# Optimization experiments

Hardware: AMD Instinct MI355X
Metric: run time of the kernel (lower is better)

The kernel has to match this reference:

```python
import jax, jax.numpy as jnp
import numpy as np

B, S, H, E, K = 4, 2048, 1024, 8, 2

def setup_inputs() -> dict:
    key = jax.random.key(0)
    k0, k1, k2, k3 = jax.random.split(key, 4)
    x = jax.random.normal(k0, (B, S, H), dtype=jnp.float32)
    # xavier-uniform-like scales
    router_w = jax.random.normal(k1, (E, H), dtype=jnp.float32) * np.float32(1.0 / np.sqrt(H))
    xav1 = np.float32(np.sqrt(2.0 / (2 * H + H)))
    w1 = jax.random.normal(k2, (E, 2 * H, H), dtype=jnp.float32) * xav1
    w2 = jax.random.normal(k3, (E, H, 2 * H), dtype=jnp.float32) * xav1
    return {"x": x, "router_w": router_w, "w1": w1, "w2": w2}

def reference(x, router_w, w1, w2):
    bsz, seq, hidden = x.shape
    n_experts = w1.shape[0]
    tokens = x.reshape(-1, hidden)                      # [T, H]
    T = tokens.shape[0]
    logits = tokens @ router_w.T                        # [T, E]
    topv, topi = jax.lax.top_k(logits, K)               # [T, K]
    w = jax.nn.softmax(topv, axis=-1).astype(tokens.dtype)
    # Dense gate matrix: gate[t, e] = routing weight of expert e for token t
    # (zero for non-selected experts). Equivalent to the torch pad/dispatch/
    # scatter-add combine: padded slots have weight 0 and contribute nothing.
    gate = jnp.zeros((T, n_experts), tokens.dtype).at[jnp.arange(T)[:, None], topi].add(w)
    out = jnp.zeros_like(tokens)
    for e in range(n_experts):  # small fixed expert count
        h = jax.nn.gelu(tokens @ w1[e].T, approximate=False)  # [T, 2H] (torch F.gelu = erf)
        y = h @ w2[e].T                                       # [T, H]
        out = out + gate[:, e:e + 1] * y
    return out.reshape(bsz, seq, hidden)
```

## Files before the change

### kernel.cpp

```cpp
#include <hip/hip_runtime.h>
#include <stdint.h>
#include <math.h>

#define T_TOK 8192
#define H_DIM 1024
#define H2    2048
#define NE    8

typedef unsigned short u16;
typedef __attribute__((ext_vector_type(8))) short bf16x8;
typedef __attribute__((ext_vector_type(4))) float f32x4;

__device__ __forceinline__ u16 f32_to_bf16(float f) {
  union { float f; unsigned u; } c; c.f = f;
  unsigned u = c.u + 0x7fffu + ((c.u >> 16) & 1u);
  return (u16)(u >> 16);
}
__device__ __forceinline__ float bf2f(u16 v) {
  union { unsigned u; float f; } c; c.u = (unsigned)v << 16; return c.f;
}

__device__ __forceinline__ float fast_gelu(float v) {
  float u = v * v;
  float z2 = v * fmaf(u, 0.1029437f, 2.3022078f);
  float e = __builtin_amdgcn_exp2f(z2);
  float r = __builtin_amdgcn_rcpf(1.0f + e);
  return v - v * r;
}

__device__ __forceinline__ void g2l16(const void* g, void* l) {
  __builtin_amdgcn_global_load_lds(
      (const __attribute__((address_space(1))) unsigned*)g,
      (__attribute__((address_space(3))) unsigned*)l, 16, 0, 0);
}

__device__ __forceinline__ int prefix_base(const int* counts, int e) {
  int b = 0;
#pragma unroll
  for (int j = 0; j < NE; j++) b += (j < e) ? counts[j] : 0;
  return b;
}

__global__ __launch_bounds__(256) void prep_kernel(
    const float* __restrict__ x, const float* __restrict__ rw,
    const float* __restrict__ w1, const float* __restrict__ w2,
    u16* __restrict__ xb, u16* __restrict__ w1b, u16* __restrict__ w2b,
    int* __restrict__ tope, float2* __restrict__ gate2,
    int* __restrict__ counts) {
  int blk = blockIdx.x;
  if (blk < T_TOK / 4) {
    int wave = threadIdx.x >> 6;
    int lane = threadIdx.x & 63;
    int t = blk * 4 + wave;
    const float4* x4 = (const float4*)(x + (size_t)t * H_DIM);
    const float4* rw4 = (const float4*)rw;
    u16* xbrow = xb + (size_t)t * H_DIM;

    double acc[NE];
#pragma unroll
    for (int e = 0; e < NE; e++) acc[e] = 0.0;
#pragma unroll
    for (int i = 0; i < 4; i++) {
      int c = lane + 64 * i;
      float4 xv = x4[c];
      ushort4 bv = make_ushort4(f32_to_bf16(xv.x), f32_to_bf16(xv.y),
                                f32_to_bf16(xv.z), f32_to_bf16(xv.w));
      *(ushort4*)(xbrow + c * 4) = bv;
#pragma unroll
      for (int e = 0; e < NE; e++) {
        float4 wv = rw4[e * 256 + c];
        acc[e] += (double)xv.x * wv.x + (double)xv.y * wv.y +
                  (double)xv.z * wv.z + (double)xv.w * wv.w;
      }
    }
#pragma unroll
    for (int off = 32; off >= 1; off >>= 1)
#pragma unroll
      for (int e = 0; e < NE; e++) acc[e] += __shfl_xor(acc[e], off, 64);

    if (lane == 0) {
      int e0 = 0; double v0 = acc[0];
#pragma unroll
      for (int e = 1; e < NE; e++) if (acc[e] > v0) { v0 = acc[e]; e0 = e; }
      int e1 = -1; double v1 = -1e300;
#pragma unroll
      for (int e = 0; e < NE; e++) if (e != e0 && acc[e] > v1) { v1 = acc[e]; e1 = e; }
      double ex = exp(v1 - v0);
      tope[t] = e0 | (e1 << 8);
      gate2[t] = make_float2((float)(1.0 / (1.0 + ex)), (float)(ex / (1.0 + ex)));
    }
  } else {
    int cb = blk - T_TOK / 4;
    if (cb == 0 && threadIdx.x < NE) counts[threadIdx.x] = 0;
    const float* src; u16* dst;
    if (cb < 3072) { src = w1; dst = w1b; }
    else           { src = w2; dst = w2b; cb -= 3072; }
    const int n4 = NE * H2 * H_DIM / 4;
    const int stride = 3072 * 256;
    const float4* s4 = (const float4*)src;
    for (int i = cb * 256 + threadIdx.x; i < n4; i += stride) {
      float4 v = s4[i];
      *(ushort4*)(dst + (size_t)i * 4) = make_ushort4(
          f32_to_bf16(v.x), f32_to_bf16(v.y), f32_to_bf16(v.z), f32_to_bf16(v.w));
    }
  }
}

__global__ __launch_bounds__(256) void build_kernel(
    const int* __restrict__ tope, int* __restrict__ counts,
    int* __restrict__ tok_list, int2* __restrict__ pos2) {
  __shared__ int cts[4][NE];
  __shared__ int gbase[NE];
  int tid = threadIdx.x, lane = tid & 63, w = tid >> 6;
  int t = blockIdx.x * 256 + tid;
  int pk = tope[t];
  int e0 = pk & 0xff, e1 = (pk >> 8) & 0xff;
  unsigned long long lt = ((unsigned long long)1 << lane) - 1;

  int r0 = 0, r1 = 0;
#pragma unroll
  for (int e = 0; e < NE; e++) {
    unsigned long long b0 = __ballot(e0 == e);
    unsigned long long b1 = __ballot(e1 == e);
    int n0 = __popcll(b0), n1 = __popcll(b1);
    if (e0 == e) r0 = __popcll(b0 & lt);
    if (e1 == e) r1 = n0 + __popcll(b1 & lt);
    if (lane == 0) cts[w][e] = n0 + n1;
  }
  __syncthreads();
  if (tid < NE) {
    int bt = cts[0][tid] + cts[1][tid] + cts[2][tid] + cts[3][tid];
    gbase[tid] = atomicAdd(&counts[tid], bt);
  }
  __syncthreads();
  int off0 = gbase[e0] + r0;
  int off1 = gbase[e1] + r1;
#pragma unroll
  for (int wp = 0; wp < 4; wp++) {
    if (wp < w) { off0 += cts[wp][e0]; off1 += cts[wp][e1]; }
  }
  tok_list[e0 * T_TOK + off0] = t;
  tok_list[e1 * T_TOK + off1] = t;
  pos2[t] = make_int2(off0, off1);
}

template <int NKT, int NT, int OUTN, bool GATHER, bool GELU>
__global__ __launch_bounds__(512, 2) void moe_gemm(
    const u16* __restrict__ A, const u16* __restrict__ W,
    u16* __restrict__ O, const int* __restrict__ tok_list,
    const int* __restrict__ counts) {
  int e = blockIdx.x & 7;
  int rem = blockIdx.x >> 3;
  int mt = rem / NT, nt = rem % NT;
  int cnt = counts[e];
  int m0 = mt * 256;
  if (m0 >= cnt) return;
  int base = prefix_base(counts, e);
  const int K = NKT * 64;

  __shared__ u16 lA[2][16384];
  __shared__ u16 lB[2][16384];

  int tid = threadIdx.x;
  int ln = tid & 63, w = tid >> 6;
  int wr = w >> 2, wc = w & 3;
  int quad = ln >> 4, l16 = ln & 15;

  const u16* We = W + (size_t)e * OUTN * K;
  const u16* aptr[4]; const u16* bptr[4];
#pragma unroll
  for (int c = 0; c < 4; ++c) {
    int u = c * 512 + tid;
    int row = u >> 3;
    int chunk = (u & 7) ^ (row & 7);
    int ar = m0 + row; if (ar > cnt - 1) ar = cnt - 1;
    const u16* ab;
    if (GATHER) ab = A + (size_t)tok_list[e * T_TOK + ar] * K;
    else        ab = A + (size_t)(base + ar) * K;
    aptr[c] = ab + chunk * 8;
    bptr[c] = We + (size_t)(nt * 256 + row) * K + chunk * 8;
  }

  int adA[8][2], adB[4][2];
#pragma unroll
  for (int f = 0; f < 8; ++f) {
    int r = wr * 128 + f * 16 + l16;
#pragma unroll
    for (int kk = 0; kk < 2; ++kk)
      adA[f][kk] = r * 64 + ((((kk << 2) | quad) ^ (r & 7)) << 3);
  }
#pragma unroll
  for (int j = 0; j < 4; ++j) {
    int r = wc * 64 + j * 16 + l16;
#pragma unroll
    for (int kk = 0; kk < 2; ++kk)
      adB[j][kk] = r * 64 + ((((kk << 2) | quad) ^ (r & 7)) << 3);
  }

  f32x4 acc[8][4];
#pragma unroll
  for (int i = 0; i < 8; i++)
#pragma unroll
    for (int j = 0; j < 4; j++)
#pragma unroll
      for (int r = 0; r < 4; r++) acc[i][j][r] = 0.f;

#pragma unroll
  for (int c = 0; c < 4; ++c) {
    g2l16(aptr[c], &lA[0][(c * 512 + tid) * 8]);
    g2l16(bptr[c], &lB[0][(c * 512 + tid) * 8]);
  }

#pragma unroll 1
  for (int t = 0; t < NKT; ++t) {
    int d = t & 1;
    asm volatile("s_waitcnt vmcnt(0)" ::: "memory");
    __builtin_amdgcn_s_barrier();
    __builtin_amdgcn_sched_barrier(0);

    const u16* Ab = &lA[d][0];
    const u16* Bb = &lB[d][0];
    bf16x8 af[8], af2[8], bf[4], bf2v[4];
    af[0]  = *(const bf16x8*)(Ab + adA[0][0]);
    af2[0] = *(const bf16x8*)(Ab + adA[0][1]);
#pragma unroll
    for (int j = 0; j < 4; ++j) {
      bf[j]   = *(const bf16x8*)(Bb + adB[j][0]);
      bf2v[j] = *(const bf16x8*)(Bb + adB[j][1]);
    }
#pragma unroll
    for (int f = 1; f < 8; ++f) {
      af[f]  = *(const bf16x8*)(Ab + adA[f][0]);
      af2[f] = *(const bf16x8*)(Ab + adA[f][1]);
    }

    if (t + 1 < NKT) {
#pragma unroll
      for (int c = 0; c < 4; ++c) {
        g2l16(aptr[c] + (t + 1) * 64, &lA[d ^ 1][(c * 512 + tid) * 8]);
        g2l16(bptr[c] + (t + 1) * 64, &lB[d ^ 1][(c * 512 + tid) * 8]);
      }
    }
    __builtin_amdgcn_sched_barrier(0);

    __builtin_amdgcn_s_setprio(1);
#pragma unroll
    for (int mi = 0; mi < 8; ++mi) {
#pragma unroll
      for (int ni = 0; ni < 4; ++ni)
        acc[mi][ni] = __builtin_amdgcn_mfma_f32_16x16x32_bf16(
            af[mi], bf[ni], acc[mi][ni], 0, 0, 0);
#pragma unroll
      for (int ni = 0; ni < 4; ++ni)
        acc[mi][ni] = __builtin_amdgcn_mfma_f32_16x16x32_bf16(
            af2[mi], bf2v[ni], acc[mi][ni], 0, 0, 0);
    }
    __builtin_amdgcn_s_setprio(0);
  }

#pragma unroll
  for (int mi = 0; mi < 8; ++mi) {
    int rb = wr * 128 + mi * 16 + quad * 4;
#pragma unroll
    for (int r = 0; r < 4; ++r) {
      int grow = m0 + rb + r;
      if (grow < cnt) {
        size_t o = (size_t)(base + grow) * OUTN + nt * 256 + wc * 64 + l16;
#pragma unroll
        for (int ni = 0; ni < 4; ++ni) {
          float v = acc[mi][ni][r];
          if (GELU) v = fast_gelu(v);
          O[o + ni * 16] = f32_to_bf16(v);
        }
      }
    }
  }
}

__global__ __launch_bounds__(256) void combine_kernel(
    const u16* __restrict__ y, const int* __restrict__ tope,
    const float2* __restrict__ gate2, const int2* __restrict__ pos2,
    const int* __restrict__ counts, float* __restrict__ out) {
  int t = blockIdx.x;
  int pk = tope[t];
  int e0 = pk & 0xff, e1 = (pk >> 8) & 0xff;
  float2 g = gate2[t];
  int2 p = pos2[t];
  int hb0 = prefix_base(counts, e0);
  int hb1 = prefix_base(counts, e1);
  size_t s0 = (size_t)(hb0 + p.x) * H_DIM + threadIdx.x * 4;
  size_t s1 = (size_t)(hb1 + p.y) * H_DIM + threadIdx.x * 4;
  ushort4 a = *(const ushort4*)(y + s0);
  ushort4 b = *(const ushort4*)(y + s1);
  float4 o;
  o.x = g.x * bf2f(a.x) + g.y * bf2f(b.x);
  o.y = g.x * bf2f(a.y) + g.y * bf2f(b.y);
  o.z = g.x * bf2f(a.z) + g.y * bf2f(b.z);
  o.w = g.x * bf2f(a.w) + g.y * bf2f(b.w);
  *(float4*)(out + (size_t)t * H_DIM + threadIdx.x * 4) = o;
}

extern "C" void kernel_launch(void* const* d_in, const int* in_sizes, int n_in,
                              void* d_out, int out_size, void* d_ws, size_t ws_size,
                              hipStream_t stream) {
  const float* x  = (const float*)d_in[0];
  const float* rw = (const float*)d_in[1];
  const float* w1 = (const float*)d_in[2];
  const float* w2 = (const float*)d_in[3];
  float* out = (float*)d_out;

  char* ws = (char*)d_ws;
  u16* xb       = (u16*)(ws);
  u16* w1b      = (u16*)(ws + 16777216);
  u16* y        = (u16*)(ws + 16777216);
  u16* w2b      = (u16*)(ws + 50331648);
  u16* h        = (u16*)(ws + 83886080);
  int* tok_list = (int*)(ws + 150994944);
  int* tope     = (int*)(ws + 151257088);
  float2* gate2 = (float2*)(ws + 151289856);
  int2* pos2    = (int2*)(ws + 151355392);
  int* counts   = (int*)(ws + 151420928);

  prep_kernel<<<T_TOK / 4 + 6144, 256, 0, stream>>>(x, rw, w1, w2, xb, w1b, w2b,
                                                    tope, gate2, counts);
  build_kernel<<<T_TOK / 256, 256, 0, stream>>>(tope, counts, tok_list, pos2);
  moe_gemm<16, 8, H2, true, true>
      <<<NE * 32 * 8, 512, 0, stream>>>(xb, w1b, h, tok_list, counts);
  moe_gemm<32, 4, H_DIM, false, false>
      <<<NE * 32 * 4, 512, 0, stream>>>(h, w2b, y, tok_list, counts);
  combine_kernel<<<T_TOK, 256, 0, stream>>>(y, tope, gate2, pos2, counts, out);
}
```

Before: 390.7 us.

## Fuse fp32-to-bf16 weight conversion into GEMM loads and split-K second GEMM

Drops the separate pass that converted w1/w2 to bf16. Each GEMM now reads fp32 weights directly into registers, packs them to bf16 and writes them into swizzled LDS, with the store deferred until after the MFMAs so it overlaps compute. The second GEMM is split into two K halves written to separate buffers, and the combine kernel sums both halves. This avoids writing and rereading bf16 weight copies and doubles the block count of the second GEMM, at the cost of fp32 weight traffic inside the GEMMs, extra partial-output traffic, and register pressure.

```diff
diff --git a/kernel.cpp b/kernel.cpp
--- a/kernel.cpp
+++ b/kernel.cpp
@@ -18,6 +18,12 @@
 }
 __device__ __forceinline__ float bf2f(u16 v) {
   union { unsigned u; float f; } c; c.u = (unsigned)v << 16; return c.f;
+}
+__device__ __forceinline__ unsigned pk_bf16(float lo, float hi) {
+  union { float f; unsigned u; } a, b; a.f = lo; b.f = hi;
+  unsigned ua = a.u + 0x7fffu + ((a.u >> 16) & 1u);
+  unsigned ub = b.u + 0x7fffu + ((b.u >> 16) & 1u);
+  return (ua >> 16) | (ub & 0xffff0000u);
 }
 
 __device__ __forceinline__ float fast_gelu(float v) {
@@ -43,66 +49,49 @@
 
 __global__ __launch_bounds__(256) void prep_kernel(
     const float* __restrict__ x, const float* __restrict__ rw,
-    const float* __restrict__ w1, const float* __restrict__ w2,
-    u16* __restrict__ xb, u16* __restrict__ w1b, u16* __restrict__ w2b,
-    int* __restrict__ tope, float2* __restrict__ gate2,
+    u16* __restrict__ xb, int* __restrict__ tope, float2* __restrict__ gate2,
     int* __restrict__ counts) {
   int blk = blockIdx.x;
-  if (blk < T_TOK / 4) {
-    int wave = threadIdx.x >> 6;
-    int lane = threadIdx.x & 63;
-    int t = blk * 4 + wave;
-    const float4* x4 = (const float4*)(x + (size_t)t * H_DIM);
-    const float4* rw4 = (const float4*)rw;
-    u16* xbrow = xb + (size_t)t * H_DIM;
-
-    double acc[NE];
-#pragma unroll
-    for (int e = 0; e < NE; e++) acc[e] = 0.0;
-#pragma unroll
-    for (int i = 0; i < 4; i++) {
-      int c = lane + 64 * i;
-      float4 xv = x4[c];
-      ushort4 bv = make_ushort4(f32_to_bf16(xv.x), f32_to_bf16(xv.y),
-                                f32_to_bf16(xv.z), f32_to_bf16(xv.w));
-      *(ushort4*)(xbrow + c * 4) = bv;
-#pragma unroll
-      for (int e = 0; e < NE; e++) {
-        float4 wv = rw4[e * 256 + c];
-        acc[e] += (double)xv.x * wv.x + (double)xv.y * wv.y +
-                  (double)xv.z * wv.z + (double)xv.w * wv.w;
-      }
-    }
-#pragma unroll
-    for (int off = 32; off >= 1; off >>= 1)
-#pragma unroll
-      for (int e = 0; e < NE; e++) acc[e] += __shfl_xor(acc[e], off, 64);
-
-    if (lane == 0) {
-      int e0 = 0; double v0 = acc[0];
-#pragma unroll
-      for (int e = 1; e < NE; e++) if (acc[e] > v0) { v0 = acc[e]; e0 = e; }
-      int e1 = -1; double v1 = -1e300;
-#pragma unroll
-      for (int e = 0; e < NE; e++) if (e != e0 && acc[e] > v1) { v1 = acc[e]; e1 = e; }
-      double ex = exp(v1 - v0);
-      tope[t] = e0 | (e1 << 8);
-      gate2[t] = make_float2((float)(1.0 / (1.0 + ex)), (float)(ex / (1.0 + ex)));
-    }
-  } else {
-    int cb = blk - T_TOK / 4;
-    if (cb == 0 && threadIdx.x < NE) counts[threadIdx.x] = 0;
-    const float* src; u16* dst;
-    if (cb < 3072) { src = w1; dst = w1b; }
-    else           { src = w2; dst = w2b; cb -= 3072; }
-    const int n4 = NE * H2 * H_DIM / 4;
-    const int stride = 3072 * 256;
-    const float4* s4 = (const float4*)src;
-    for (int i = cb * 256 + threadIdx.x; i < n4; i += stride) {
-      float4 v = s4[i];
-      *(ushort4*)(dst + (size_t)i * 4) = make_ushort4(
-          f32_to_bf16(v.x), f32_to_bf16(v.y), f32_to_bf16(v.z), f32_to_bf16(v.w));
-    }
+  if (blk == 0 && threadIdx.x < NE) counts[threadIdx.x] = 0;
+  int wave = threadIdx.x >> 6;
+  int lane = threadIdx.x & 63;
+  int t = blk * 4 + wave;
+  const float4* x4 = (const float4*)(x + (size_t)t * H_DIM);
+  const float4* rw4 = (const float4*)rw;
+  u16* xbrow = xb + (size_t)t * H_DIM;
+
+  double acc[NE];
+#pragma unroll
+  for (int e = 0; e < NE; e++) acc[e] = 0.0;
+#pragma unroll
+  for (int i = 0; i < 4; i++) {
+    int c = lane + 64 * i;
+    float4 xv = x4[c];
+    ushort4 bv = make_ushort4(f32_to_bf16(xv.x), f32_to_bf16(xv.y),
+                              f32_to_bf16(xv.z), f32_to_bf16(xv.w));
+    *(ushort4*)(xbrow + c * 4) = bv;
+#pragma unroll
+    for (int e = 0; e < NE; e++) {
+      float4 wv = rw4[e * 256 + c];
+      acc[e] += (double)xv.x * wv.x + (double)xv.y * wv.y +
+                (double)xv.z * wv.z + (double)xv.w * wv.w;
+    }
+  }
+#pragma unroll
+  for (int off = 32; off >= 1; off >>= 1)
+#pragma unroll
+    for (int e = 0; e < NE; e++) acc[e] += __shfl_xor(acc[e], off, 64);
+
+  if (lane == 0) {
+    int e0 = 0; double v0 = acc[0];
+#pragma unroll
+    for (int e = 1; e < NE; e++) if (acc[e] > v0) { v0 = acc[e]; e0 = e; }
+    int e1 = -1; double v1 = -1e300;
+#pragma unroll
+    for (int e = 0; e < NE; e++) if (e != e0 && acc[e] > v1) { v1 = acc[e]; e1 = e; }
+    double ex = exp(v1 - v0);
+    tope[t] = e0 | (e1 << 8);
+    gate2[t] = make_float2((float)(1.0 / (1.0 + ex)), (float)(ex / (1.0 + ex)));
   }
 }
 
@@ -144,19 +133,23 @@
   pos2[t] = make_int2(off0, off1);
 }
 
-template <int NKT, int NT, int OUTN, bool GATHER, bool GELU>
+template <int NKT, int NT, int KFULL, int KSPLIT, int OUTN, bool GATHER, bool GELU>
 __global__ __launch_bounds__(512, 2) void moe_gemm(
-    const u16* __restrict__ A, const u16* __restrict__ W,
+    const u16* __restrict__ A, const float* __restrict__ Wf,
     u16* __restrict__ O, const int* __restrict__ tok_list,
     const int* __restrict__ counts) {
   int e = blockIdx.x & 7;
   int rem = blockIdx.x >> 3;
-  int mt = rem / NT, nt = rem % NT;
+  int nt = rem % NT;
+  int mtk = rem / NT;
+  int mt = mtk & 31;
+  int kh = mtk >> 5;
   int cnt = counts[e];
   int m0 = mt * 256;
   if (m0 >= cnt) return;
   int base = prefix_base(counts, e);
-  const int K = NKT * 64;
+  const int k0 = kh * NKT * 64;
+  O += (size_t)kh * 2 * T_TOK * OUTN;
 
   __shared__ u16 lA[2][16384];
   __shared__ u16 lB[2][16384];
@@ -166,8 +159,7 @@
   int wr = w >> 2, wc = w & 3;
   int quad = ln >> 4, l16 = ln & 15;
 
-  const u16* We = W + (size_t)e * OUTN * K;
-  const u16* aptr[4]; const u16* bptr[4];
+  const u16* aptr[4];
 #pragma unroll
   for (int c = 0; c < 4; ++c) {
     int u = c * 512 + tid;
@@ -175,11 +167,16 @@
     int chunk = (u & 7) ^ (row & 7);
     int ar = m0 + row; if (ar > cnt - 1) ar = cnt - 1;
     const u16* ab;
-    if (GATHER) ab = A + (size_t)tok_list[e * T_TOK + ar] * K;
-    else        ab = A + (size_t)(base + ar) * K;
-    aptr[c] = ab + chunk * 8;
-    bptr[c] = We + (size_t)(nt * 256 + row) * K + chunk * 8;
-  }
+    if (GATHER) ab = A + (size_t)tok_list[e * T_TOK + ar] * KFULL;
+    else        ab = A + (size_t)(base + ar) * KFULL;
+    aptr[c] = ab + k0 + chunk * 8;
+  }
+
+  const int rB = tid >> 1, hf = tid & 1;
+  const float4* bsrc = (const float4*)(
+      Wf + (size_t)e * OUTN * KFULL + (size_t)(nt * 256 + rB) * KFULL +
+      k0 + hf * 32);
+  const int rB7 = rB & 7, hf4 = hf * 4;
 
   int adA[8][2], adB[4][2];
 #pragma unroll
@@ -205,18 +202,39 @@
 #pragma unroll
       for (int r = 0; r < 4; r++) acc[i][j][r] = 0.f;
 
-#pragma unroll
-  for (int c = 0; c < 4; ++c) {
-    g2l16(aptr[c], &lA[0][(c * 512 + tid) * 8]);
-    g2l16(bptr[c], &lB[0][(c * 512 + tid) * 8]);
+  {
+    float4 bv[8];
+#pragma unroll
+    for (int j = 0; j < 8; ++j) bv[j] = bsrc[j];
+#pragma unroll
+    for (int c = 0; c < 4; ++c) g2l16(aptr[c], &lA[0][(c * 512 + tid) * 8]);
+    u16* wb = &lB[0][rB * 64];
+#pragma unroll
+    for (int j2 = 0; j2 < 4; ++j2) {
+      uint4 pk;
+      pk.x = pk_bf16(bv[2 * j2].x, bv[2 * j2].y);
+      pk.y = pk_bf16(bv[2 * j2].z, bv[2 * j2].w);
+      pk.z = pk_bf16(bv[2 * j2 + 1].x, bv[2 * j2 + 1].y);
+      pk.w = pk_bf16(bv[2 * j2 + 1].z, bv[2 * j2 + 1].w);
+      *(uint4*)(wb + (((hf4 + j2) ^ rB7) << 3)) = pk;
+    }
   }
 
 #pragma unroll 1
   for (int t = 0; t < NKT; ++t) {
     int d = t & 1;
-    asm volatile("s_waitcnt vmcnt(0)" ::: "memory");
+    asm volatile("s_waitcnt vmcnt(0) lgkmcnt(0)" ::: "memory");
     __builtin_amdgcn_s_barrier();
     __builtin_amdgcn_sched_barrier(0);
+
+    float4 bv[8];
+    if (t + 1 < NKT) {
+#pragma unroll
+      for (int j = 0; j < 8; ++j) bv[j] = bsrc[(t + 1) * 16 + j];
+#pragma unroll
+      for (int c = 0; c < 4; ++c)
+        g2l16(aptr[c] + (t + 1) * 64, &lA[d ^ 1][(c * 512 + tid) * 8]);
+    }
 
     const u16* Ab = &lA[d][0];
     const u16* Bb = &lB[d][0];
@@ -234,15 +252,6 @@
       af2[f] = *(const bf16x8*)(Ab + adA[f][1]);
     }
 
-    if (t + 1 < NKT) {
-#pragma unroll
-      for (int c = 0; c < 4; ++c) {
-        g2l16(aptr[c] + (t + 1) * 64, &lA[d ^ 1][(c * 512 + tid) * 8]);
-        g2l16(bptr[c] + (t + 1) * 64, &lB[d ^ 1][(c * 512 + tid) * 8]);
-      }
-    }
-    __builtin_amdgcn_sched_barrier(0);
-
     __builtin_amdgcn_s_setprio(1);
 #pragma unroll
     for (int mi = 0; mi < 8; ++mi) {
@@ -256,6 +265,20 @@
             af2[mi], bf2v[ni], acc[mi][ni], 0, 0, 0);
     }
     __builtin_amdgcn_s_setprio(0);
+    __builtin_amdgcn_sched_barrier(0);
+
+    if (t + 1 < NKT) {
+      u16* wb = &lB[d ^ 1][rB * 64];
+#pragma unroll
+      for (int j2 = 0; j2 < 4; ++j2) {
+        uint4 pk;
+        pk.x = pk_bf16(bv[2 * j2].x, bv[2 * j2].y);
+        pk.y = pk_bf16(bv[2 * j2].z, bv[2 * j2].w);
+        pk.z = pk_bf16(bv[2 * j2 + 1].x, bv[2 * j2 + 1].y);
+        pk.w = pk_bf16(bv[2 * j2 + 1].z, bv[2 * j2 + 1].w);
+        *(uint4*)(wb + (((hf4 + j2) ^ rB7) << 3)) = pk;
+      }
+    }
   }
 
 #pragma unroll
@@ -281,6 +304,7 @@
     const u16* __restrict__ y, const int* __restrict__ tope,
     const float2* __restrict__ gate2, const int2* __restrict__ pos2,
     const int* __restrict__ counts, float* __restrict__ out) {
+  const u16* y1 = y + (size_t)2 * T_TOK * H_DIM;
   int t = blockIdx.x;
   int pk = tope[t];
   int e0 = pk & 0xff, e1 = (pk >> 8) & 0xff;
@@ -290,13 +314,15 @@
   int hb1 = prefix_base(counts, e1);
   size_t s0 = (size_t)(hb0 + p.x) * H_DIM + threadIdx.x * 4;
   size_t s1 = (size_t)(hb1 + p.y) * H_DIM + threadIdx.x * 4;
-  ushort4 a = *(const ushort4*)(y + s0);
-  ushort4 b = *(const ushort4*)(y + s1);
+  ushort4 a0 = *(const ushort4*)(y + s0);
+  ushort4 a1 = *(const ushort4*)(y1 + s0);
+  ushort4 b0 = *(const ushort4*)(y + s1);
+  ushort4 b1 = *(const ushort4*)(y1 + s1);
   float4 o;
-  o.x = g.x * bf2f(a.x) + g.y * bf2f(b.x);
-  o.y = g.x * bf2f(a.y) + g.y * bf2f(b.y);
-  o.z = g.x * bf2f(a.z) + g.y * bf2f(b.z);
-  o.w = g.x * bf2f(a.w) + g.y * bf2f(b.w);
+  o.x = g.x * (bf2f(a0.x) + bf2f(a1.x)) + g.y * (bf2f(b0.x) + bf2f(b1.x));
+  o.y = g.x * (bf2f(a0.y) + bf2f(a1.y)) + g.y * (bf2f(b0.y) + bf2f(b1.y));
+  o.z = g.x * (bf2f(a0.z) + bf2f(a1.z)) + g.y * (bf2f(b0.z) + bf2f(b1.z));
+  o.w = g.x * (bf2f(a0.w) + bf2f(a1.w)) + g.y * (bf2f(b0.w) + bf2f(b1.w));
   *(float4*)(out + (size_t)t * H_DIM + threadIdx.x * 4) = o;
 }
 
@@ -311,22 +337,19 @@
 
   char* ws = (char*)d_ws;
   u16* xb       = (u16*)(ws);
-  u16* w1b      = (u16*)(ws + 16777216);
-  u16* y        = (u16*)(ws + 16777216);
-  u16* w2b      = (u16*)(ws + 50331648);
-  u16* h        = (u16*)(ws + 83886080);
+  u16* h        = (u16*)(ws + 16777216);
+  u16* y        = (u16*)(ws + 83886080);
   int* tok_list = (int*)(ws + 150994944);
   int* tope     = (int*)(ws + 151257088);
   float2* gate2 = (float2*)(ws + 151289856);
   int2* pos2    = (int2*)(ws + 151355392);
   int* counts   = (int*)(ws + 151420928);
 
-  prep_kernel<<<T_TOK / 4 + 6144, 256, 0, stream>>>(x, rw, w1, w2, xb, w1b, w2b,
-                                                    tope, gate2, counts);
+  prep_kernel<<<T_TOK / 4, 256, 0, stream>>>(x, rw, xb, tope, gate2, counts);
   build_kernel<<<T_TOK / 256, 256, 0, stream>>>(tope, counts, tok_list, pos2);
-  moe_gemm<16, 8, H2, true, true>
-      <<<NE * 32 * 8, 512, 0, stream>>>(xb, w1b, h, tok_list, counts);
-  moe_gemm<32, 4, H_DIM, false, false>
-      <<<NE * 32 * 4, 512, 0, stream>>>(h, w2b, y, tok_list, counts);
+  moe_gemm<16, 8, 1024, 1, H2, true, true>
+      <<<NE * 32 * 8, 512, 0, stream>>>(xb, w1, h, tok_list, counts);
+  moe_gemm<16, 4, 2048, 2, H_DIM, false, false>
+      <<<NE * 32 * 4 * 2, 512, 0, stream>>>(h, w2, y, tok_list, counts);
   combine_kernel<<<T_TOK, 256, 0, stream>>>(y, tope, gate2, pos2, counts, out);
 }
```

After: 1.120 ms. 2.87x slower.

## Shrink GEMM tiles to 128x256 with K=32 steps and overlap w2 conversion with GEMM1

Applied to the files above, without the earlier changes.

The w2 fp32-to-bf16 conversion moves out of the prep kernel and into extra blocks of the first expert GEMM launch, so it runs alongside the w1 GEMM. The GEMM tile changes from 256x256 with 512 threads and K=64 per stage to 128x256 with 256 threads and K=32 per stage, with a new paired-row swizzled LDS layout. The goal is less padding waste on the ragged per-expert token counts, more blocks and a smaller LDS footprint. The cost is lower arithmetic intensity per block, twice as many barriers per K, and conversion blocks that compete with GEMM blocks for CUs.

```diff
diff --git a/kernel.cpp b/kernel.cpp
--- a/kernel.cpp
+++ b/kernel.cpp
@@ -43,8 +43,8 @@
 
 __global__ __launch_bounds__(256) void prep_kernel(
     const float* __restrict__ x, const float* __restrict__ rw,
-    const float* __restrict__ w1, const float* __restrict__ w2,
-    u16* __restrict__ xb, u16* __restrict__ w1b, u16* __restrict__ w2b,
+    const float* __restrict__ w1,
+    u16* __restrict__ xb, u16* __restrict__ w1b,
     int* __restrict__ tope, float2* __restrict__ gate2,
     int* __restrict__ counts) {
   int blk = blockIdx.x;
@@ -92,15 +92,12 @@
   } else {
     int cb = blk - T_TOK / 4;
     if (cb == 0 && threadIdx.x < NE) counts[threadIdx.x] = 0;
-    const float* src; u16* dst;
-    if (cb < 3072) { src = w1; dst = w1b; }
-    else           { src = w2; dst = w2b; cb -= 3072; }
     const int n4 = NE * H2 * H_DIM / 4;
     const int stride = 3072 * 256;
-    const float4* s4 = (const float4*)src;
+    const float4* s4 = (const float4*)w1;
     for (int i = cb * 256 + threadIdx.x; i < n4; i += stride) {
       float4 v = s4[i];
-      *(ushort4*)(dst + (size_t)i * 4) = make_ushort4(
+      *(ushort4*)(w1b + (size_t)i * 4) = make_ushort4(
           f32_to_bf16(v.x), f32_to_bf16(v.y), f32_to_bf16(v.z), f32_to_bf16(v.w));
     }
   }
@@ -144,57 +141,70 @@
   pos2[t] = make_int2(off0, off1);
 }
 
-template <int NKT, int NT, int OUTN, bool GATHER, bool GELU>
-__global__ __launch_bounds__(512, 2) void moe_gemm(
+template <int NKT, int NT, int KFULL, int OUTN, bool GATHER, bool GELU, bool CVT>
+__global__ __launch_bounds__(256, 2) void moe_gemm(
     const u16* __restrict__ A, const u16* __restrict__ W,
     u16* __restrict__ O, const int* __restrict__ tok_list,
-    const int* __restrict__ counts) {
+    const int* __restrict__ counts,
+    const float* __restrict__ cvt_src, u16* __restrict__ cvt_dst) {
+  if (CVT && blockIdx.x >= 8 * 64 * NT) {
+    int cb = blockIdx.x - 8 * 64 * NT;
+    const int n4 = NE * H2 * H_DIM / 4;
+    const float4* s4 = (const float4*)cvt_src;
+    for (int i = cb * 256 + threadIdx.x; i < n4; i += 1024 * 256) {
+      float4 v = s4[i];
+      *(ushort4*)(cvt_dst + (size_t)i * 4) = make_ushort4(
+          f32_to_bf16(v.x), f32_to_bf16(v.y), f32_to_bf16(v.z), f32_to_bf16(v.w));
+    }
+    return;
+  }
   int e = blockIdx.x & 7;
   int rem = blockIdx.x >> 3;
   int mt = rem / NT, nt = rem % NT;
   int cnt = counts[e];
-  int m0 = mt * 256;
+  int m0 = mt * 128;
   if (m0 >= cnt) return;
   int base = prefix_base(counts, e);
-  const int K = NKT * 64;
-
-  __shared__ u16 lA[2][16384];
-  __shared__ u16 lB[2][16384];
+
+  __shared__ u16 lA[2][4096];
+  __shared__ u16 lB[2][8192];
 
   int tid = threadIdx.x;
   int ln = tid & 63, w = tid >> 6;
-  int wr = w >> 2, wc = w & 3;
+  int wc = w;
   int quad = ln >> 4, l16 = ln & 15;
 
-  const u16* We = W + (size_t)e * OUTN * K;
-  const u16* aptr[4]; const u16* bptr[4];
-#pragma unroll
-  for (int c = 0; c < 4; ++c) {
-    int u = c * 512 + tid;
-    int row = u >> 3;
-    int chunk = (u & 7) ^ (row & 7);
-    int ar = m0 + row; if (ar > cnt - 1) ar = cnt - 1;
+  const u16* We = W + (size_t)e * OUTN * KFULL;
+  const u16* aptr[2]; const u16* bptr[4];
+#pragma unroll
+  for (int c2 = 0; c2 < 2; ++c2) {
+    int u = c2 * 256 + tid;
+    int lr = u >> 3, l = (u & 7) ^ (lr & 7);
+    int r = lr * 2 + (l >> 2), c = l & 3;
+    int ar = m0 + r; if (ar > cnt - 1) ar = cnt - 1;
     const u16* ab;
-    if (GATHER) ab = A + (size_t)tok_list[e * T_TOK + ar] * K;
-    else        ab = A + (size_t)(base + ar) * K;
-    aptr[c] = ab + chunk * 8;
-    bptr[c] = We + (size_t)(nt * 256 + row) * K + chunk * 8;
-  }
-
-  int adA[8][2], adB[4][2];
+    if (GATHER) ab = A + (size_t)tok_list[e * T_TOK + ar] * KFULL;
+    else        ab = A + (size_t)(base + ar) * KFULL;
+    aptr[c2] = ab + c * 8;
+  }
+#pragma unroll
+  for (int c2 = 0; c2 < 4; ++c2) {
+    int u = c2 * 256 + tid;
+    int lr = u >> 3, l = (u & 7) ^ (lr & 7);
+    int r = lr * 2 + (l >> 2), c = l & 3;
+    bptr[c2] = We + (size_t)(nt * 256 + r) * KFULL + c * 8;
+  }
+
+  int adA[8], adB[4];
 #pragma unroll
   for (int f = 0; f < 8; ++f) {
-    int r = wr * 128 + f * 16 + l16;
-#pragma unroll
-    for (int kk = 0; kk < 2; ++kk)
-      adA[f][kk] = r * 64 + ((((kk << 2) | quad) ^ (r & 7)) << 3);
+    int r = f * 16 + l16;
+    adA[f] = (r >> 1) * 64 + ((((r & 1) * 4 + quad) ^ ((r >> 1) & 7)) << 3);
   }
 #pragma unroll
   for (int j = 0; j < 4; ++j) {
     int r = wc * 64 + j * 16 + l16;
-#pragma unroll
-    for (int kk = 0; kk < 2; ++kk)
-      adB[j][kk] = r * 64 + ((((kk << 2) | quad) ^ (r & 7)) << 3);
+    adB[j] = (r >> 1) * 64 + ((((r & 1) * 4 + quad) ^ ((r >> 1) & 7)) << 3);
   }
 
   f32x4 acc[8][4];
@@ -206,10 +216,9 @@
       for (int r = 0; r < 4; r++) acc[i][j][r] = 0.f;
 
 #pragma unroll
-  for (int c = 0; c < 4; ++c) {
-    g2l16(aptr[c], &lA[0][(c * 512 + tid) * 8]);
-    g2l16(bptr[c], &lB[0][(c * 512 + tid) * 8]);
-  }
+  for (int c2 = 0; c2 < 2; ++c2) g2l16(aptr[c2], &lA[0][(c2 * 256 + tid) * 8]);
+#pragma unroll
+  for (int c2 = 0; c2 < 4; ++c2) g2l16(bptr[c2], &lB[0][(c2 * 256 + tid) * 8]);
 
 #pragma unroll 1
   for (int t = 0; t < NKT; ++t) {
@@ -218,49 +227,36 @@
     __builtin_amdgcn_s_barrier();
     __builtin_amdgcn_sched_barrier(0);
 
-    const u16* Ab = &lA[d][0];
-    const u16* Bb = &lB[d][0];
-    bf16x8 af[8], af2[8], bf[4], bf2v[4];
-    af[0]  = *(const bf16x8*)(Ab + adA[0][0]);
-    af2[0] = *(const bf16x8*)(Ab + adA[0][1]);
-#pragma unroll
-    for (int j = 0; j < 4; ++j) {
-      bf[j]   = *(const bf16x8*)(Bb + adB[j][0]);
-      bf2v[j] = *(const bf16x8*)(Bb + adB[j][1]);
-    }
-#pragma unroll
-    for (int f = 1; f < 8; ++f) {
-      af[f]  = *(const bf16x8*)(Ab + adA[f][0]);
-      af2[f] = *(const bf16x8*)(Ab + adA[f][1]);
-    }
-
     if (t + 1 < NKT) {
 #pragma unroll
-      for (int c = 0; c < 4; ++c) {
-        g2l16(aptr[c] + (t + 1) * 64, &lA[d ^ 1][(c * 512 + tid) * 8]);
-        g2l16(bptr[c] + (t + 1) * 64, &lB[d ^ 1][(c * 512 + tid) * 8]);
-      }
-    }
+      for (int c2 = 0; c2 < 2; ++c2)
+        g2l16(aptr[c2] + (t + 1) * 32, &lA[d ^ 1][(c2 * 256 + tid) * 8]);
+#pragma unroll
+      for (int c2 = 0; c2 < 4; ++c2)
+        g2l16(bptr[c2] + (t + 1) * 32, &lB[d ^ 1][(c2 * 256 + tid) * 8]);
+    }
+
+    bf16x8 af[8], bf[4];
+    af[0] = *(const bf16x8*)(&lA[d][0] + adA[0]);
+#pragma unroll
+    for (int j = 0; j < 4; ++j) bf[j] = *(const bf16x8*)(&lB[d][0] + adB[j]);
+#pragma unroll
+    for (int f = 1; f < 8; ++f) af[f] = *(const bf16x8*)(&lA[d][0] + adA[f]);
     __builtin_amdgcn_sched_barrier(0);
 
     __builtin_amdgcn_s_setprio(1);
 #pragma unroll
-    for (int mi = 0; mi < 8; ++mi) {
+    for (int mi = 0; mi < 8; ++mi)
 #pragma unroll
       for (int ni = 0; ni < 4; ++ni)
         acc[mi][ni] = __builtin_amdgcn_mfma_f32_16x16x32_bf16(
             af[mi], bf[ni], acc[mi][ni], 0, 0, 0);
-#pragma unroll
-      for (int ni = 0; ni < 4; ++ni)
-        acc[mi][ni] = __builtin_amdgcn_mfma_f32_16x16x32_bf16(
-            af2[mi], bf2v[ni], acc[mi][ni], 0, 0, 0);
-    }
     __builtin_amdgcn_s_setprio(0);
   }
 
 #pragma unroll
   for (int mi = 0; mi < 8; ++mi) {
-    int rb = wr * 128 + mi * 16 + quad * 4;
+    int rb = mi * 16 + quad * 4;
 #pragma unroll
     for (int r = 0; r < 4; ++r) {
       int grow = m0 + rb + r;
@@ -321,12 +317,14 @@
   int2* pos2    = (int2*)(ws + 151355392);
   int* counts   = (int*)(ws + 151420928);
 
-  prep_kernel<<<T_TOK / 4 + 6144, 256, 0, stream>>>(x, rw, w1, w2, xb, w1b, w2b,
+  prep_kernel<<<T_TOK / 4 + 3072, 256, 0, stream>>>(x, rw, w1, xb, w1b,
                                                     tope, gate2, counts);
   build_kernel<<<T_TOK / 256, 256, 0, stream>>>(tope, counts, tok_list, pos2);
-  moe_gemm<16, 8, H2, true, true>
-      <<<NE * 32 * 8, 512, 0, stream>>>(xb, w1b, h, tok_list, counts);
-  moe_gemm<32, 4, H_DIM, false, false>
-      <<<NE * 32 * 4, 512, 0, stream>>>(h, w2b, y, tok_list, counts);
+  moe_gemm<32, 8, 1024, H2, true, true, true>
+      <<<8 * 64 * 8 + 1024, 256, 0, stream>>>(xb, w1b, h, tok_list, counts,
+                                              w2, w2b);
+  moe_gemm<64, 4, 2048, H_DIM, false, false, false>
+      <<<8 * 64 * 4, 256, 0, stream>>>(h, w2b, y, tok_list, counts,
+                                       nullptr, nullptr);
   combine_kernel<<<T_TOK, 256, 0, stream>>>(y, tope, gate2, pos2, counts, out);
 }
```

Measured after the change: 418.8 us. +7.2%, slower.

## Fuse fp32-to-bf16 weight conversion into MoE GEMM B-tile loads

Applied to the files above, without the earlier changes.

Removes the separate prep pass that converted w1/w2 to bf16. The GEMMs now stream fp32 weights straight into LDS and convert them to bf16 in registers before the MFMAs. The K tile shrinks from 64 to 32 to make room for fp32 in LDS, occupancy drops to one block per CU, and the prefetch is issued before the LDS reads. This trades the conversion pass's extra global traffic for twice the weight bytes per GEMM tile, plus the cost of reading each weight row once per M-tile and converting it every time.

```diff
diff --git a/kernel.cpp b/kernel.cpp
--- a/kernel.cpp
+++ b/kernel.cpp
@@ -10,6 +10,7 @@
 typedef unsigned short u16;
 typedef __attribute__((ext_vector_type(8))) short bf16x8;
 typedef __attribute__((ext_vector_type(4))) float f32x4;
+typedef __attribute__((ext_vector_type(4))) unsigned int u32x4;
 
 __device__ __forceinline__ u16 f32_to_bf16(float f) {
   union { float f; unsigned u; } c; c.f = f;
@@ -18,6 +19,12 @@
 }
 __device__ __forceinline__ float bf2f(u16 v) {
   union { unsigned u; float f; } c; c.u = (unsigned)v << 16; return c.f;
+}
+__device__ __forceinline__ unsigned pk_bf16(float lo, float hi) {
+  union { float f; unsigned u; } a, b; a.f = lo; b.f = hi;
+  unsigned ua = a.u + 0x7fffu + ((a.u >> 16) & 1u);
+  unsigned ub = b.u + 0x7fffu + ((b.u >> 16) & 1u);
+  return (ua >> 16) | (ub & 0xffff0000u);
 }
 
 __device__ __forceinline__ float fast_gelu(float v) {
@@ -43,66 +50,49 @@
 
 __global__ __launch_bounds__(256) void prep_kernel(
     const float* __restrict__ x, const float* __restrict__ rw,
-    const float* __restrict__ w1, const float* __restrict__ w2,
-    u16* __restrict__ xb, u16* __restrict__ w1b, u16* __restrict__ w2b,
-    int* __restrict__ tope, float2* __restrict__ gate2,
+    u16* __restrict__ xb, int* __restrict__ tope, float2* __restrict__ gate2,
     int* __restrict__ counts) {
   int blk = blockIdx.x;
-  if (blk < T_TOK / 4) {
-    int wave = threadIdx.x >> 6;
-    int lane = threadIdx.x & 63;
-    int t = blk * 4 + wave;
-    const float4* x4 = (const float4*)(x + (size_t)t * H_DIM);
-    const float4* rw4 = (const float4*)rw;
-    u16* xbrow = xb + (size_t)t * H_DIM;
-
-    double acc[NE];
-#pragma unroll
-    for (int e = 0; e < NE; e++) acc[e] = 0.0;
-#pragma unroll
-    for (int i = 0; i < 4; i++) {
-      int c = lane + 64 * i;
-      float4 xv = x4[c];
-      ushort4 bv = make_ushort4(f32_to_bf16(xv.x), f32_to_bf16(xv.y),
-                                f32_to_bf16(xv.z), f32_to_bf16(xv.w));
-      *(ushort4*)(xbrow + c * 4) = bv;
-#pragma unroll
-      for (int e = 0; e < NE; e++) {
-        float4 wv = rw4[e * 256 + c];
-        acc[e] += (double)xv.x * wv.x + (double)xv.y * wv.y +
-                  (double)xv.z * wv.z + (double)xv.w * wv.w;
-      }
-    }
-#pragma unroll
-    for (int off = 32; off >= 1; off >>= 1)
-#pragma unroll
-      for (int e = 0; e < NE; e++) acc[e] += __shfl_xor(acc[e], off, 64);
-
-    if (lane == 0) {
-      int e0 = 0; double v0 = acc[0];
-#pragma unroll
-      for (int e = 1; e < NE; e++) if (acc[e] > v0) { v0 = acc[e]; e0 = e; }
-      int e1 = -1; double v1 = -1e300;
-#pragma unroll
-      for (int e = 0; e < NE; e++) if (e != e0 && acc[e] > v1) { v1 = acc[e]; e1 = e; }
-      double ex = exp(v1 - v0);
-      tope[t] = e0 | (e1 << 8);
-      gate2[t] = make_float2((float)(1.0 / (1.0 + ex)), (float)(ex / (1.0 + ex)));
-    }
-  } else {
-    int cb = blk - T_TOK / 4;
-    if (cb == 0 && threadIdx.x < NE) counts[threadIdx.x] = 0;
-    const float* src; u16* dst;
-    if (cb < 3072) { src = w1; dst = w1b; }
-    else           { src = w2; dst = w2b; cb -= 3072; }
-    const int n4 = NE * H2 * H_DIM / 4;
-    const int stride = 3072 * 256;
-    const float4* s4 = (const float4*)src;
-    for (int i = cb * 256 + threadIdx.x; i < n4; i += stride) {
-      float4 v = s4[i];
-      *(ushort4*)(dst + (size_t)i * 4) = make_ushort4(
-          f32_to_bf16(v.x), f32_to_bf16(v.y), f32_to_bf16(v.z), f32_to_bf16(v.w));
-    }
+  if (blk == 0 && threadIdx.x < NE) counts[threadIdx.x] = 0;
+  int wave = threadIdx.x >> 6;
+  int lane = threadIdx.x & 63;
+  int t = blk * 4 + wave;
+  const float4* x4 = (const float4*)(x + (size_t)t * H_DIM);
+  const float4* rw4 = (const float4*)rw;
+  u16* xbrow = xb + (size_t)t * H_DIM;
+
+  double acc[NE];
+#pragma unroll
+  for (int e = 0; e < NE; e++) acc[e] = 0.0;
+#pragma unroll
+  for (int i = 0; i < 4; i++) {
+    int c = lane + 64 * i;
+    float4 xv = x4[c];
+    ushort4 bv = make_ushort4(f32_to_bf16(xv.x), f32_to_bf16(xv.y),
+                              f32_to_bf16(xv.z), f32_to_bf16(xv.w));
+    *(ushort4*)(xbrow + c * 4) = bv;
+#pragma unroll
+    for (int e = 0; e < NE; e++) {
+      float4 wv = rw4[e * 256 + c];
+      acc[e] += (double)xv.x * wv.x + (double)xv.y * wv.y +
+                (double)xv.z * wv.z + (double)xv.w * wv.w;
+    }
+  }
+#pragma unroll
+  for (int off = 32; off >= 1; off >>= 1)
+#pragma unroll
+    for (int e = 0; e < NE; e++) acc[e] += __shfl_xor(acc[e], off, 64);
+
+  if (lane == 0) {
+    int e0 = 0; double v0 = acc[0];
+#pragma unroll
+    for (int e = 1; e < NE; e++) if (acc[e] > v0) { v0 = acc[e]; e0 = e; }
+    int e1 = -1; double v1 = -1e300;
+#pragma unroll
+    for (int e = 0; e < NE; e++) if (e != e0 && acc[e] > v1) { v1 = acc[e]; e1 = e; }
+    double ex = exp(v1 - v0);
+    tope[t] = e0 | (e1 << 8);
+    gate2[t] = make_float2((float)(1.0 / (1.0 + ex)), (float)(ex / (1.0 + ex)));
   }
 }
 
@@ -145,10 +135,11 @@
 }
 
 template <int NKT, int NT, int OUTN, bool GATHER, bool GELU>
-__global__ __launch_bounds__(512, 2) void moe_gemm(
-    const u16* __restrict__ A, const u16* __restrict__ W,
+__global__ __launch_bounds__(512, 1) void moe_gemm(
+    const u16* __restrict__ A, const float* __restrict__ Wf,
     u16* __restrict__ O, const int* __restrict__ tok_list,
     const int* __restrict__ counts) {
+  const int K = NKT * 32;
   int e = blockIdx.x & 7;
   int rem = blockIdx.x >> 3;
   int mt = rem / NT, nt = rem % NT;
@@ -156,45 +147,48 @@
   int m0 = mt * 256;
   if (m0 >= cnt) return;
   int base = prefix_base(counts, e);
-  const int K = NKT * 64;
-
-  __shared__ u16 lA[2][16384];
-  __shared__ u16 lB[2][16384];
+
+  __shared__ u16 lA[2][8192];
+  __shared__ float lB[2][8192];
 
   int tid = threadIdx.x;
   int ln = tid & 63, w = tid >> 6;
   int wr = w >> 2, wc = w & 3;
   int quad = ln >> 4, l16 = ln & 15;
 
-  const u16* We = W + (size_t)e * OUTN * K;
-  const u16* aptr[4]; const u16* bptr[4];
-#pragma unroll
-  for (int c = 0; c < 4; ++c) {
-    int u = c * 512 + tid;
-    int row = u >> 3;
-    int chunk = (u & 7) ^ (row & 7);
+  const u16* aptr[2];
+#pragma unroll
+  for (int c2 = 0; c2 < 2; ++c2) {
+    int u = c2 * 512 + tid;
+    int row = u >> 2, lg = (u & 3) ^ (row & 3);
     int ar = m0 + row; if (ar > cnt - 1) ar = cnt - 1;
     const u16* ab;
     if (GATHER) ab = A + (size_t)tok_list[e * T_TOK + ar] * K;
     else        ab = A + (size_t)(base + ar) * K;
-    aptr[c] = ab + chunk * 8;
-    bptr[c] = We + (size_t)(nt * 256 + row) * K + chunk * 8;
-  }
-
-  int adA[8][2], adB[4][2];
+    aptr[c2] = ab + lg * 8;
+  }
+  const float* We = Wf + (size_t)e * OUTN * K;
+  const float* bptr[4];
+#pragma unroll
+  for (int c2 = 0; c2 < 4; ++c2) {
+    int u = c2 * 512 + tid;
+    int row = u >> 3, lg = (u & 7) ^ (row & 7);
+    bptr[c2] = We + (size_t)(nt * 256 + row) * K + lg * 4;
+  }
+
+  int adA[8];
 #pragma unroll
   for (int f = 0; f < 8; ++f) {
     int r = wr * 128 + f * 16 + l16;
-#pragma unroll
-    for (int kk = 0; kk < 2; ++kk)
-      adA[f][kk] = r * 64 + ((((kk << 2) | quad) ^ (r & 7)) << 3);
-  }
+    adA[f] = r * 32 + ((quad ^ (r & 3)) << 3);
+  }
+  int adB[4][2];
 #pragma unroll
   for (int j = 0; j < 4; ++j) {
     int r = wc * 64 + j * 16 + l16;
 #pragma unroll
-    for (int kk = 0; kk < 2; ++kk)
-      adB[j][kk] = r * 64 + ((((kk << 2) | quad) ^ (r & 7)) << 3);
+    for (int s = 0; s < 2; ++s)
+      adB[j][s] = r * 32 + ((((quad << 1) | s) ^ (r & 7)) << 2);
   }
 
   f32x4 acc[8][4];
@@ -206,10 +200,9 @@
       for (int r = 0; r < 4; r++) acc[i][j][r] = 0.f;
 
 #pragma unroll
-  for (int c = 0; c < 4; ++c) {
-    g2l16(aptr[c], &lA[0][(c * 512 + tid) * 8]);
-    g2l16(bptr[c], &lB[0][(c * 512 + tid) * 8]);
-  }
+  for (int c2 = 0; c2 < 2; ++c2) g2l16(aptr[c2], &lA[0][(c2 * 512 + tid) * 8]);
+#pragma unroll
+  for (int c2 = 0; c2 < 4; ++c2) g2l16(bptr[c2], &lB[0][(c2 * 512 + tid) * 4]);
 
 #pragma unroll 1
   for (int t = 0; t < NKT; ++t) {
@@ -218,43 +211,44 @@
     __builtin_amdgcn_s_barrier();
     __builtin_amdgcn_sched_barrier(0);
 
-    const u16* Ab = &lA[d][0];
-    const u16* Bb = &lB[d][0];
-    bf16x8 af[8], af2[8], bf[4], bf2v[4];
-    af[0]  = *(const bf16x8*)(Ab + adA[0][0]);
-    af2[0] = *(const bf16x8*)(Ab + adA[0][1]);
+    if (t + 1 < NKT) {
+#pragma unroll
+      for (int c2 = 0; c2 < 2; ++c2)
+        g2l16(aptr[c2] + (t + 1) * 32, &lA[d ^ 1][(c2 * 512 + tid) * 8]);
+#pragma unroll
+      for (int c2 = 0; c2 < 4; ++c2)
+        g2l16(bptr[c2] + (t + 1) * 32, &lB[d ^ 1][(c2 * 512 + tid) * 4]);
+    }
+
+    bf16x8 af[8];
+    float4 b0[4], b1[4];
 #pragma unroll
     for (int j = 0; j < 4; ++j) {
-      bf[j]   = *(const bf16x8*)(Bb + adB[j][0]);
-      bf2v[j] = *(const bf16x8*)(Bb + adB[j][1]);
-    }
-#pragma unroll
-    for (int f = 1; f < 8; ++f) {
-      af[f]  = *(const bf16x8*)(Ab + adA[f][0]);
-      af2[f] = *(const bf16x8*)(Ab + adA[f][1]);
-    }
-
-    if (t + 1 < NKT) {
-#pragma unroll
-      for (int c = 0; c < 4; ++c) {
-        g2l16(aptr[c] + (t + 1) * 64, &lA[d ^ 1][(c * 512 + tid) * 8]);
-        g2l16(bptr[c] + (t + 1) * 64, &lB[d ^ 1][(c * 512 + tid) * 8]);
-      }
-    }
+      b0[j] = *(const float4*)(&lB[d][0] + adB[j][0]);
+      b1[j] = *(const float4*)(&lB[d][0] + adB[j][1]);
+    }
+#pragma unroll
+    for (int f = 0; f < 8; ++f) af[f] = *(const bf16x8*)(&lA[d][0] + adA[f]);
     __builtin_amdgcn_sched_barrier(0);
 
+    bf16x8 bf[4];
+#pragma unroll
+    for (int j = 0; j < 4; ++j) {
+      union { bf16x8 h; u32x4 u; } cv;
+      cv.u.x = pk_bf16(b0[j].x, b0[j].y);
+      cv.u.y = pk_bf16(b0[j].z, b0[j].w);
+      cv.u.z = pk_bf16(b1[j].x, b1[j].y);
+      cv.u.w = pk_bf16(b1[j].z, b1[j].w);
+      bf[j] = cv.h;
+    }
+
     __builtin_amdgcn_s_setprio(1);
 #pragma unroll
-    for (int mi = 0; mi < 8; ++mi) {
+    for (int mi = 0; mi < 8; ++mi)
 #pragma unroll
       for (int ni = 0; ni < 4; ++ni)
         acc[mi][ni] = __builtin_amdgcn_mfma_f32_16x16x32_bf16(
             af[mi], bf[ni], acc[mi][ni], 0, 0, 0);
-#pragma unroll
-      for (int ni = 0; ni < 4; ++ni)
-        acc[mi][ni] = __builtin_amdgcn_mfma_f32_16x16x32_bf16(
-            af2[mi], bf2v[ni], acc[mi][ni], 0, 0, 0);
-    }
     __builtin_amdgcn_s_setprio(0);
   }
 
@@ -311,22 +305,19 @@
 
   char* ws = (char*)d_ws;
   u16* xb       = (u16*)(ws);
-  u16* w1b      = (u16*)(ws + 16777216);
-  u16* y        = (u16*)(ws + 16777216);
-  u16* w2b      = (u16*)(ws + 50331648);
-  u16* h        = (u16*)(ws + 83886080);
-  int* tok_list = (int*)(ws + 150994944);
-  int* tope     = (int*)(ws + 151257088);
-  float2* gate2 = (float2*)(ws + 151289856);
-  int2* pos2    = (int2*)(ws + 151355392);
-  int* counts   = (int*)(ws + 151420928);
-
-  prep_kernel<<<T_TOK / 4 + 6144, 256, 0, stream>>>(x, rw, w1, w2, xb, w1b, w2b,
-                                                    tope, gate2, counts);
+  u16* h        = (u16*)(ws + 16777216);
+  u16* y        = (u16*)(ws + 83886080);
+  int* tok_list = (int*)(ws + 117440512);
+  int* tope     = (int*)(ws + 117702656);
+  float2* gate2 = (float2*)(ws + 117735424);
+  int2* pos2    = (int2*)(ws + 117800960);
+  int* counts   = (int*)(ws + 117866496);
+
+  prep_kernel<<<T_TOK / 4, 256, 0, stream>>>(x, rw, xb, tope, gate2, counts);
   build_kernel<<<T_TOK / 256, 256, 0, stream>>>(tope, counts, tok_list, pos2);
-  moe_gemm<16, 8, H2, true, true>
-      <<<NE * 32 * 8, 512, 0, stream>>>(xb, w1b, h, tok_list, counts);
-  moe_gemm<32, 4, H_DIM, false, false>
-      <<<NE * 32 * 4, 512, 0, stream>>>(h, w2b, y, tok_list, counts);
+  moe_gemm<32, 8, H2, true, true>
+      <<<8 * 32 * 8, 512, 0, stream>>>(xb, w1, h, tok_list, counts);
+  moe_gemm<64, 4, H_DIM, false, false>
+      <<<8 * 32 * 4, 512, 0, stream>>>(h, w2, y, tok_list, counts);
   combine_kernel<<<T_TOK, 256, 0, stream>>>(y, tope, gate2, pos2, counts, out);
 }
```

After: 585.7 us. +49.9%, slower.
